# Performance work log

Hardware: AMD Instinct MI355X
Metric: run time of the kernel (lower is better)

The kernel has to match this reference:

```python
import jax, jax.numpy as jnp
import numpy as np

N_NODES = 32
GAT_OUT = 64
LSTM_H = 128
N_CLS = 4
NEG_SLOPE = 0.2


def setup_inputs() -> dict:
    key = jax.random.key(0)
    ks = jax.random.split(key, 12)
    B, T, E = 32, 512, 96
    F, H = GAT_OUT, LSTM_H
    s = 0.05
    return {
        "x_seq": jax.random.normal(ks[0], (B, T, N_NODES), jnp.float32),
        "edge_index": jax.random.randint(ks[1], (2, E), 0, N_NODES, jnp.int32),
        # GATConv params (heads=1): lin weight [in=1, F], attention vectors [F], bias [F]
        "w_gat": jax.random.normal(ks[2], (1, F), jnp.float32) * s,
        "att_src": jax.random.normal(ks[3], (F,), jnp.float32) * s,
        "att_dst": jax.random.normal(ks[4], (F,), jnp.float32) * s,
        "b_gat": jnp.zeros((F,), jnp.float32),
        # LSTM params, torch gate order (i, f, g, o)
        "W_ih": jax.random.normal(ks[5], (N_NODES * F, 4 * H), jnp.float32) * s,
        "W_hh": jax.random.normal(ks[6], (H, 4 * H), jnp.float32) * s,
        "b_ih": jnp.zeros((4 * H,), jnp.float32),
        "b_hh": jnp.zeros((4 * H,), jnp.float32),
        # classifier
        "W_fc": jax.random.normal(ks[7], (H, N_CLS), jnp.float32) * s,
        "b_fc": jnp.zeros((N_CLS,), jnp.float32),
    }


def _forward(x_seq, edge_index, w_gat, att_src, att_dst, b_gat,
             W_ih, W_hh, b_ih, b_hh, W_fc, b_fc):
    B, T, N = x_seq.shape
    F = w_gat.shape[1]
    H = W_hh.shape[0]

    # --- GAT over all (B,T) steps at once (PyG GATConv, heads=1, self-loops) ---
    loops = jnp.arange(N, dtype=edge_index.dtype)
    src = jnp.concatenate([edge_index[0], loops])  # [Et]
    dst = jnp.concatenate([edge_index[1], loops])  # [Et]
    Et = src.shape[0]

    h = x_seq[..., None] * w_gat            # [B,T,N,F] (in_channels=1 linear)
    a_s = h @ att_src                        # [B,T,N]
    a_d = h @ att_dst                        # [B,T,N]
    e = a_s[..., src] + a_d[..., dst]        # [B,T,Et]
    e = jnp.where(e > 0, e, NEG_SLOPE * e)   # LeakyReLU(0.2)

    # segment softmax over destination node, batched over B*T
    e2 = jnp.moveaxis(e, -1, 0).reshape(Et, B * T)
    m = jax.ops.segment_max(e2, dst, num_segments=N)        # [N,B*T]
    ex = jnp.exp(e2 - m[dst])
    z = jax.ops.segment_sum(ex, dst, num_segments=N)        # [N,B*T]
    alpha = ex / z[dst]                                      # [Et,B*T]
    alpha = jnp.moveaxis(alpha.reshape(Et, B, T), 0, -1)     # [B,T,Et]

    msg = alpha[..., None] * h[:, :, src, :]                 # [B,T,Et,F]
    onehot = (dst[:, None] == jnp.arange(N)).astype(h.dtype)  # [Et,N]
    out = jnp.einsum('btef,en->btnf', msg, onehot) + b_gat    # [B,T,N,F]

    seq = out.reshape(B, T, N * F)           # [B,T,2048]

    # --- single-layer LSTM (batch_first), torch gate order i,f,g,o ---
    xw = seq @ W_ih + (b_ih + b_hh)          # [B,T,4H]

    def step(carry, xw_t):
        hs, cs = carry
        g = xw_t + hs @ W_hh                 # [B,4H]
        i, f, gg, o = jnp.split(g, 4, axis=-1)
        cs = jax.nn.sigmoid(f) * cs + jax.nn.sigmoid(i) * jnp.tanh(gg)
        hs = jax.nn.sigmoid(o) * jnp.tanh(cs)
        return (hs, cs), None

    h0 = jnp.zeros((B, H), seq.dtype)
    (h_last, _), _ = jax.lax.scan(step, (h0, h0), jnp.moveaxis(xw, 1, 0))

    return h_last @ W_fc + b_fc              # [B,num_classes]


def reference(x_seq, edge_index, w_gat, att_src, att_dst, b_gat,
              W_ih, W_hh, b_ih, b_hh, W_fc, b_fc):
    return _forward(x_seq, edge_index, w_gat, att_src, att_dst, b_gat,
                    W_ih, W_hh, b_ih, b_hh, W_fc, b_fc)
```

## Files before the change

### kernel.cpp

```cpp
#include <hip/hip_runtime.h>

#define NN 32
#define FF 64
#define HH 128
#define G4 512
#define BB 32
#define TT 512
#define ET 128
#define NPOS (BB*TT)

__device__ __forceinline__ float frcp(float x) { return __builtin_amdgcn_rcpf(x); }

__global__ __launch_bounds__(512) void prep_kernel(const float* __restrict__ w_gat,
                                                   const float* __restrict__ b_gat,
                                                   const float* __restrict__ W_ih,
                                                   const float* __restrict__ W_hh,
                                                   float* __restrict__ W_eff,
                                                   float* __restrict__ biasp,
                                                   float* __restrict__ Wt) {
  int j = threadIdx.x;
  int n = blockIdx.x;
  float accw = 0.f, accb = 0.f;
#pragma unroll 8
  for (int f = 0; f < FF; ++f) {
    float wv = W_ih[(n * FF + f) * G4 + j];
    accw = fmaf(w_gat[f], wv, accw);
    accb = fmaf(b_gat[f], wv, accb);
  }
  W_eff[n * G4 + j] = accw;
  biasp[n * G4 + j] = accb;
  int g0 = (n * G4 + j) * 4;
#pragma unroll
  for (int q = 0; q < 4; ++q) {
    int e = g0 + q;
    int tl = e >> 7, idx = e & 127;
    int r = tl >> 2, kq = tl & 3;
    int g = idx >> 5, kk = idx & 31;
    Wt[e] = W_hh[(kq * 32 + kk) * G4 + g * 128 + r];
  }
}

__global__ __launch_bounds__(256) void gatxw_kernel(const float* __restrict__ x_seq,
                                                    const int* __restrict__ ei,
                                                    const float* __restrict__ w_gat,
                                                    const float* __restrict__ att_src,
                                                    const float* __restrict__ att_dst,
                                                    const float* __restrict__ b_ih,
                                                    const float* __restrict__ b_hh,
                                                    const float* __restrict__ W_eff,
                                                    const float* __restrict__ biasp,
                                                    float* __restrict__ xw) {
  __shared__ int srt[ET];
  __shared__ int offs[NN + 1];
  __shared__ int cnt[NN];
  __shared__ float xs[256];
  __shared__ float sl[256];
  __shared__ float scal_sh[2];
  int tid = threadIdx.x;
  int posbase = blockIdx.x * 8;
  float we0[NN], we1[NN];
#pragma unroll
  for (int nn = 0; nn < NN; ++nn) {
    we0[nn] = W_eff[nn * G4 + tid];
    we1[nn] = W_eff[nn * G4 + 256 + tid];
  }
  float b0 = b_ih[tid] + b_hh[tid];
  float b1 = b_ih[256 + tid] + b_hh[256 + tid];
#pragma unroll 8
  for (int n = 0; n < NN; ++n) {
    b0 += biasp[n * G4 + tid];
    b1 += biasp[n * G4 + 256 + tid];
  }
  if (tid < NN) cnt[tid] = 0;
  __syncthreads();
  int es = 0, ed = 0, tk = 0;
  if (tid < ET) {
    if (tid < 96) { es = ei[tid]; ed = ei[96 + tid]; }
    else { es = tid - 96; ed = tid - 96; }
    tk = atomicAdd(&cnt[ed], 1);
  }
  __syncthreads();
  if (tid == 0) {
    offs[0] = 0;
    for (int n = 0; n < NN; ++n) offs[n + 1] = offs[n] + cnt[n];
  }
  if (tid == 1) {
    float cs = 0.f, cd = 0.f;
    for (int f = 0; f < FF; ++f) {
      cs = fmaf(w_gat[f], att_src[f], cs);
      cd = fmaf(w_gat[f], att_dst[f], cd);
    }
    scal_sh[0] = cs;
    scal_sh[1] = cd;
  }
  __syncthreads();
  if (tid < ET) srt[offs[ed] + tk] = es;
  xs[tid] = x_seq[posbase * NN + tid];
  __syncthreads();
  float cs = scal_sh[0], cd = scal_sh[1];
  int p = tid >> 5, n = tid & 31;
  int base = p * 32;
  int e0 = offs[n], e1 = offs[n + 1];
  float xn = xs[base + n];
  float cdxn = cd * xn;
  float m = -3.0e38f;
  for (int e = e0; e < e1; ++e) {
    float ev = fmaf(cs, xs[base + srt[e]], cdxn);
    ev = ev > 0.f ? ev : 0.2f * ev;
    m = fmaxf(m, ev);
  }
  float z = 0.f, sa = 0.f;
  for (int e = e0; e < e1; ++e) {
    float xsv = xs[base + srt[e]];
    float ev = fmaf(cs, xsv, cdxn);
    ev = ev > 0.f ? ev : 0.2f * ev;
    float ex = __expf(ev - m);
    z += ex;
    sa = fmaf(ex, xsv, sa);
  }
  sl[p * 32 + n] = sa * frcp(z);
  __syncthreads();
  for (int pp = 0; pp < 8; ++pp) {
    const float4* sp = (const float4*)&sl[pp * 32];
    float a0 = b0, a1 = b1;
#pragma unroll
    for (int q = 0; q < 8; ++q) {
      float4 sv = sp[q];
      a0 = fmaf(sv.x, we0[4 * q], a0);
      a0 = fmaf(sv.y, we0[4 * q + 1], a0);
      a0 = fmaf(sv.z, we0[4 * q + 2], a0);
      a0 = fmaf(sv.w, we0[4 * q + 3], a0);
      a1 = fmaf(sv.x, we1[4 * q], a1);
      a1 = fmaf(sv.y, we1[4 * q + 1], a1);
      a1 = fmaf(sv.z, we1[4 * q + 2], a1);
      a1 = fmaf(sv.w, we1[4 * q + 3], a1);
    }
    size_t row = (size_t)(posbase + pp) * G4;
    xw[row + tid] = a0;
    xw[row + 256 + tid] = a1;
  }
}


#define PK16F(HP, W0, W1, W2, W3) \
  "v_pk_fma_f32 v[216:217], v[" HP "], v[" W0 "], 0\n\t" \
  "v_pk_fma_f32 v[218:219], v[" HP "], v[" W1 "], 0\n\t" \
  "v_pk_fma_f32 v[220:221], v[" HP "], v[" W2 "], 0\n\t" \
  "v_pk_fma_f32 v[222:223], v[" HP "], v[" W3 "], 0\n\t"

#define PK16A(HP, W0, W1, W2, W3) \
  "v_pk_fma_f32 v[216:217], v[" HP "], v[" W0 "], v[216:217]\n\t" \
  "v_pk_fma_f32 v[218:219], v[" HP "], v[" W1 "], v[218:219]\n\t" \
  "v_pk_fma_f32 v[220:221], v[" HP "], v[" W2 "], v[220:221]\n\t" \
  "v_pk_fma_f32 v[222:223], v[" HP "], v[" W3 "], v[222:223]\n\t"

#define PHASE(XSLOT, RD, WR) \
  "ds_read_b128 v[32:35], " RD "\n\t" \
  "ds_read_b128 v[36:39], " RD " offset:16\n\t" \
  "ds_read_b128 v[40:43], " RD " offset:32\n\t" \
  "ds_read_b128 v[44:47], " RD " offset:48\n\t" \
  "ds_read_b128 v[48:51], " RD " offset:64\n\t" \
  "ds_read_b128 v[52:55], " RD " offset:80\n\t" \
  "ds_read_b128 v[56:59], " RD " offset:96\n\t" \
  "ds_read_b128 v[60:63], " RD " offset:112\n\t" \
  "s_waitcnt lgkmcnt(7)\n\t" \
  PK16F("32:33", "64:65",  "96:97",   "128:129", "160:161") \
  PK16A("34:35", "66:67",  "98:99",   "130:131", "162:163") \
  "s_waitcnt lgkmcnt(6)\n\t" \
  PK16A("36:37", "68:69",  "100:101", "132:133", "164:165") \
  PK16A("38:39", "70:71",  "102:103", "134:135", "166:167") \
  "s_waitcnt lgkmcnt(5)\n\t" \
  PK16A("40:41", "72:73",  "104:105", "136:137", "168:169") \
  PK16A("42:43", "74:75",  "106:107", "138:139", "170:171") \
  "s_waitcnt lgkmcnt(4)\n\t" \
  PK16A("44:45", "76:77",  "108:109", "140:141", "172:173") \
  PK16A("46:47", "78:79",  "110:111", "142:143", "174:175") \
  "s_waitcnt lgkmcnt(3)\n\t" \
  PK16A("48:49", "80:81",  "112:113", "144:145", "176:177") \
  PK16A("50:51", "82:83",  "114:115", "146:147", "178:179") \
  "s_waitcnt lgkmcnt(2)\n\t" \
  PK16A("52:53", "84:85",  "116:117", "148:149", "180:181") \
  PK16A("54:55", "86:87",  "118:119", "150:151", "182:183") \
  "s_waitcnt lgkmcnt(1)\n\t" \
  PK16A("56:57", "88:89",  "120:121", "152:153", "184:185") \
  PK16A("58:59", "90:91",  "122:123", "154:155", "186:187") \
  "s_waitcnt lgkmcnt(0)\n\t" \
  PK16A("60:61", "92:93",  "124:125", "156:157", "188:189") \
  PK16A("62:63", "94:95",  "126:127", "158:159", "190:191") \
  "s_waitcnt vmcnt(3)\n\t" \
  "v_mov_b32 v215, " XSLOT "\n\t" \
  "global_load_dword " XSLOT ", v194, %[xwb]\n\t" \
  "v_add_u32 v194, 0x800, v194\n\t" \
  "v_add_f32 v204, v216, v217\n\t" \
  "v_add_f32 v205, v218, v219\n\t" \
  "v_add_f32 v206, v220, v221\n\t" \
  "v_add_f32 v207, v222, v223\n\t" \
  "v_add_f32_dpp v204, v204, v204 quad_perm:[1,0,3,2] row_mask:0xf bank_mask:0xf\n\t" \
  "v_add_f32_dpp v205, v205, v205 quad_perm:[1,0,3,2] row_mask:0xf bank_mask:0xf\n\t" \
  "v_add_f32_dpp v206, v206, v206 quad_perm:[1,0,3,2] row_mask:0xf bank_mask:0xf\n\t" \
  "v_add_f32_dpp v207, v207, v207 quad_perm:[1,0,3,2] row_mask:0xf bank_mask:0xf\n\t" \
  "v_add_f32_dpp v204, v204, v204 quad_perm:[2,3,0,1] row_mask:0xf bank_mask:0xf\n\t" \
  "v_add_f32_dpp v205, v205, v205 quad_perm:[2,3,0,1] row_mask:0xf bank_mask:0xf\n\t" \
  "v_add_f32_dpp v206, v206, v206 quad_perm:[2,3,0,1] row_mask:0xf bank_mask:0xf\n\t" \
  "v_add_f32_dpp v207, v207, v207 quad_perm:[2,3,0,1] row_mask:0xf bank_mask:0xf\n\t" \
  "v_cndmask_b32 v208, v204, v205, s[22:23]\n\t" \
  "v_cndmask_b32 v209, v206, v207, s[22:23]\n\t" \
  "v_cndmask_b32 v208, v208, v209, s[24:25]\n\t" \
  "v_add_f32 v208, v208, v215\n\t" \
  "v_mul_f32 v209, v200, v208\n\t" \
  "v_exp_f32 v209, v209\n\t" \
  "s_nop 0\n\t" \
  "v_add_f32 v209, 1.0, v209\n\t" \
  "v_rcp_f32 v209, v209\n\t" \
  "s_nop 0\n\t" \
  "v_fma_f32 v210, v201, v209, v202\n\t" \
  "s_nop 1\n\t" \
  "v_add_f32_dpp v211, v210, v203 quad_perm:[0,0,0,0] row_mask:0xf bank_mask:0xf\n\t" \
  "v_add_f32_dpp v212, v210, v203 quad_perm:[1,1,1,1] row_mask:0xf bank_mask:0xf\n\t" \
  "v_add_f32_dpp v213, v210, v203 quad_perm:[2,2,2,2] row_mask:0xf bank_mask:0xf\n\t" \
  "v_add_f32_dpp v214, v210, v203 quad_perm:[3,3,3,3] row_mask:0xf bank_mask:0xf\n\t" \
  "v_mul_f32 v211, v211, v213\n\t" \
  "v_fma_f32 v199, v212, v199, v211\n\t" \
  "v_mul_f32 v209, 0x4038aa3b, v199\n\t" \
  "v_exp_f32 v209, v209\n\t" \
  "s_nop 0\n\t" \
  "v_add_f32 v209, 1.0, v209\n\t" \
  "v_rcp_f32 v209, v209\n\t" \
  "s_nop 0\n\t" \
  "v_fma_f32 v209, -2.0, v209, 1.0\n\t" \
  "v_mul_f32 v209, v214, v209\n\t" \
  "ds_write_b32 " WR ", v209\n\t" \
  "s_waitcnt lgkmcnt(0)\n\t" \
  "s_barrier\n\t"

__global__ __launch_bounds__(512, 2) void lstm_kernel(const float* __restrict__ xw,
                                                      const float* __restrict__ Wt,
                                                      const float* __restrict__ W_fc,
                                                      const float* __restrict__ b_fc,
                                                      float* __restrict__ out) {
  __shared__ __align__(16) float lds[320];
  int b = blockIdx.x, tid = threadIdx.x;
  int r = tid >> 2, kq = tid & 3;
  if (tid < 320) lds[tid] = 0.f;
  const float* xwb = xw + (size_t)b * TT * G4;
  unsigned xoff0 = (unsigned)((kq * 128 + r) * 4);
  unsigned wtoff = (unsigned)(tid * 512);
  unsigned lbase = (unsigned)(uintptr_t)&lds[0];
  unsigned rda = lbase + kq * 160;
  unsigned rdb = rda + 640;
  unsigned wra = lbase + (((r >> 5) * 40 + (r & 31)) << 2);
  unsigned wrb = wra + 640;
  float kmulf = (kq == 2) ? __uint_as_float(0x4038aa3bu)
                          : __uint_as_float(0xbfb8aa3bu);
  float Af = (kq == 2) ? -2.f : 1.f;
  float Bf = (kq == 2) ? 1.f : 0.f;
  unsigned kqodd = kq & 1, kqhi = kq >> 1;
  __syncthreads();
  asm volatile(
    "v_mov_b32 v194, %[xo]\n\t"
    "v_mov_b32 v195, %[rda]\n\t"
    "v_mov_b32 v196, %[rdb]\n\t"
    "v_mov_b32 v197, %[wra]\n\t"
    "v_mov_b32 v198, %[wrb]\n\t"
    "v_mov_b32 v199, 0\n\t"
    "v_mov_b32 v200, %[km]\n\t"
    "v_mov_b32 v201, %[Aa]\n\t"
    "v_mov_b32 v202, %[Bb]\n\t"
    "v_mov_b32 v203, 0\n\t"
    "v_cmp_eq_u32 s[22:23], 1, %[kodd]\n\t"
    "v_cmp_eq_u32 s[24:25], 1, %[khi]\n\t"
    "global_load_dword v224, v194, %[xwb]\n\t"
    "v_add_u32 v194, 0x800, v194\n\t"
    "global_load_dword v225, v194, %[xwb]\n\t"
    "v_add_u32 v194, 0x800, v194\n\t"
    "global_load_dword v226, v194, %[xwb]\n\t"
    "v_add_u32 v194, 0x800, v194\n\t"
    "global_load_dword v227, v194, %[xwb]\n\t"
    "v_add_u32 v194, 0x800, v194\n\t"
    "global_load_dwordx4 v[64:67], %[wto], %[wtb] offset:0\n\t"
    "global_load_dwordx4 v[68:71], %[wto], %[wtb] offset:16\n\t"
    "global_load_dwordx4 v[72:75], %[wto], %[wtb] offset:32\n\t"
    "global_load_dwordx4 v[76:79], %[wto], %[wtb] offset:48\n\t"
    "global_load_dwordx4 v[80:83], %[wto], %[wtb] offset:64\n\t"
    "global_load_dwordx4 v[84:87], %[wto], %[wtb] offset:80\n\t"
    "global_load_dwordx4 v[88:91], %[wto], %[wtb] offset:96\n\t"
    "global_load_dwordx4 v[92:95], %[wto], %[wtb] offset:112\n\t"
    "global_load_dwordx4 v[96:99], %[wto], %[wtb] offset:128\n\t"
    "global_load_dwordx4 v[100:103], %[wto], %[wtb] offset:144\n\t"
    "global_load_dwordx4 v[104:107], %[wto], %[wtb] offset:160\n\t"
    "global_load_dwordx4 v[108:111], %[wto], %[wtb] offset:176\n\t"
    "global_load_dwordx4 v[112:115], %[wto], %[wtb] offset:192\n\t"
    "global_load_dwordx4 v[116:119], %[wto], %[wtb] offset:208\n\t"
    "global_load_dwordx4 v[120:123], %[wto], %[wtb] offset:224\n\t"
    "global_load_dwordx4 v[124:127], %[wto], %[wtb] offset:240\n\t"
    "global_load_dwordx4 v[128:131], %[wto], %[wtb] offset:256\n\t"
    "global_load_dwordx4 v[132:135], %[wto], %[wtb] offset:272\n\t"
    "global_load_dwordx4 v[136:139], %[wto], %[wtb] offset:288\n\t"
    "global_load_dwordx4 v[140:143], %[wto], %[wtb] offset:304\n\t"
    "global_load_dwordx4 v[144:147], %[wto], %[wtb] offset:320\n\t"
    "global_load_dwordx4 v[148:151], %[wto], %[wtb] offset:336\n\t"
    "global_load_dwordx4 v[152:155], %[wto], %[wtb] offset:352\n\t"
    "global_load_dwordx4 v[156:159], %[wto], %[wtb] offset:368\n\t"
    "global_load_dwordx4 v[160:163], %[wto], %[wtb] offset:384\n\t"
    "global_load_dwordx4 v[164:167], %[wto], %[wtb] offset:400\n\t"
    "global_load_dwordx4 v[168:171], %[wto], %[wtb] offset:416\n\t"
    "global_load_dwordx4 v[172:175], %[wto], %[wtb] offset:432\n\t"
    "global_load_dwordx4 v[176:179], %[wto], %[wtb] offset:448\n\t"
    "global_load_dwordx4 v[180:183], %[wto], %[wtb] offset:464\n\t"
    "global_load_dwordx4 v[184:187], %[wto], %[wtb] offset:480\n\t"
    "global_load_dwordx4 v[188:191], %[wto], %[wtb] offset:496\n\t"
    "s_waitcnt vmcnt(0)\n\t"
    "s_movk_i32 s20, 0x80\n\t"
    "L_lstm_%=:\n\t"
    PHASE("v224", "v195", "v198")
    PHASE("v225", "v196", "v197")
    PHASE("v226", "v195", "v198")
    PHASE("v227", "v196", "v197")
    "s_sub_u32 s20, s20, 1\n\t"
    "s_cmp_lg_u32 s20, 0\n\t"
    "s_cbranch_scc1 L_lstm_%=\n\t"
    "s_waitcnt vmcnt(0) lgkmcnt(0)\n\t"
    :
    : [xwb]"s"(xwb), [wtb]"s"(Wt), [wto]"v"(wtoff), [xo]"v"(xoff0),
      [rda]"v"(rda), [rdb]"v"(rdb), [wra]"v"(wra), [wrb]"v"(wrb),
      [km]"v"(kmulf), [Aa]"v"(Af), [Bb]"v"(Bf),
      [kodd]"v"(kqodd), [khi]"v"(kqhi)
    : "memory", "scc", "s20", "s22", "s23", "s24", "s25",
      "v32","v33","v34","v35","v36","v37","v38","v39",
      "v40","v41","v42","v43","v44","v45","v46","v47",
      "v48","v49","v50","v51","v52","v53","v54","v55",
      "v56","v57","v58","v59","v60","v61","v62","v63",
      "v64","v65","v66","v67","v68","v69","v70","v71",
      "v72","v73","v74","v75","v76","v77","v78","v79",
      "v80","v81","v82","v83","v84","v85","v86","v87",
      "v88","v89","v90","v91","v92","v93","v94","v95",
      "v96","v97","v98","v99","v100","v101","v102","v103",
      "v104","v105","v106","v107","v108","v109","v110","v111",
      "v112","v113","v114","v115","v116","v117","v118","v119",
      "v120","v121","v122","v123","v124","v125","v126","v127",
      "v128","v129","v130","v131","v132","v133","v134","v135",
      "v136","v137","v138","v139","v140","v141","v142","v143",
      "v144","v145","v146","v147","v148","v149","v150","v151",
      "v152","v153","v154","v155","v156","v157","v158","v159",
      "v160","v161","v162","v163","v164","v165","v166","v167",
      "v168","v169","v170","v171","v172","v173","v174","v175",
      "v176","v177","v178","v179","v180","v181","v182","v183",
      "v184","v185","v186","v187","v188","v189","v190","v191",
      "v192","v193","v194","v195","v196","v197","v198","v199",
      "v200","v201","v202","v203","v204","v205","v206","v207",
      "v208","v209","v210","v211","v212","v213","v214","v215",
      "v216","v217","v218","v219","v220","v221","v222","v223",
      "v224","v225","v226","v227");
  __syncthreads();
  if (tid < 4) {
    float acc = b_fc[tid];
#pragma unroll 8
    for (int k = 0; k < HH; ++k)
      acc = fmaf(lds[(k >> 5) * 40 + (k & 31)], W_fc[k * 4 + tid], acc);
    out[b * 4 + tid] = acc;
  }
}

extern "C" void kernel_launch(void* const* d_in, const int* in_sizes, int n_in,
                              void* d_out, int out_size, void* d_ws, size_t ws_size,
                              hipStream_t stream) {
  const float* x_seq   = (const float*)d_in[0];
  const int*   ei      = (const int*)d_in[1];
  const float* w_gat   = (const float*)d_in[2];
  const float* att_src = (const float*)d_in[3];
  const float* att_dst = (const float*)d_in[4];
  const float* b_gat   = (const float*)d_in[5];
  const float* W_ih    = (const float*)d_in[6];
  const float* W_hh    = (const float*)d_in[7];
  const float* b_ih    = (const float*)d_in[8];
  const float* b_hh    = (const float*)d_in[9];
  const float* W_fc    = (const float*)d_in[10];
  const float* b_fc    = (const float*)d_in[11];

  float* ws = (float*)d_ws;
  float* Wt    = ws;
  float* xw    = Wt + 65536;
  float* W_eff = xw + (size_t)(NPOS + 8) * G4;
  float* biasp = W_eff + NN * G4;

  prep_kernel<<<NN, G4, 0, stream>>>(w_gat, b_gat, W_ih, W_hh, W_eff, biasp, Wt);
  gatxw_kernel<<<NPOS / 8, 256, 0, stream>>>(x_seq, ei, w_gat, att_src, att_dst,
                                             b_ih, b_hh, W_eff, biasp, xw);
  lstm_kernel<<<BB, G4, 0, stream>>>(xw, Wt, W_fc, b_fc, (float*)d_out);
}
```

Baseline: 377.2 us.

## Share hidden-state LDS reads across lanes via DPP row rotation in LSTM step

In the LSTM recurrence, each lane now reads only 8 hidden values from LDS per step instead of 32. The other 24 values reach it through three DPP row_ror:4 rotations among neighbouring lanes. The W_hh register layout in prep_kernel is permuted so each rotated slice meets the matching weights, and the LDS hidden-state layout drops its padding. The aim is less LDS read traffic and latency on the serial per-step critical path, at the cost of 24 extra DPP moves per step and a more intricate weight permutation.

```diff
diff --git a/kernel.cpp b/kernel.cpp
--- a/kernel.cpp
+++ b/kernel.cpp
@@ -32,11 +32,17 @@
   int g0 = (n * G4 + j) * 4;
 #pragma unroll
   for (int q = 0; q < 4; ++q) {
-    int e = g0 + q;
-    int tl = e >> 7, idx = e & 127;
-    int r = tl >> 2, kq = tl & 3;
-    int g = idx >> 5, kk = idx & 31;
-    Wt[e] = W_hh[(kq * 32 + kk) * G4 + g * 128 + r];
+    int E = g0 + q;
+    int tl = E >> 7;
+    int idx = E & 127;
+    int s = idx >> 5;
+    int jj = (idx >> 3) & 3;
+    int g = (idx >> 1) & 3;
+    int e = idx & 1;
+    int r = tl >> 2, kq = tl & 3, lr = r & 3;
+    int bb = (lr - s) & 3;
+    int k = kq * 32 + 8 * bb + 2 * jj + e;
+    Wt[E] = W_hh[k * G4 + g * 128 + r];
   }
 }
 
@@ -142,51 +148,52 @@
 }
 
 
-#define PK16F(HP, W0, W1, W2, W3) \
+#define PK4F(HP, W0, W1, W2, W3) \
   "v_pk_fma_f32 v[216:217], v[" HP "], v[" W0 "], 0\n\t" \
   "v_pk_fma_f32 v[218:219], v[" HP "], v[" W1 "], 0\n\t" \
   "v_pk_fma_f32 v[220:221], v[" HP "], v[" W2 "], 0\n\t" \
   "v_pk_fma_f32 v[222:223], v[" HP "], v[" W3 "], 0\n\t"
 
-#define PK16A(HP, W0, W1, W2, W3) \
+#define PK4A(HP, W0, W1, W2, W3) \
   "v_pk_fma_f32 v[216:217], v[" HP "], v[" W0 "], v[216:217]\n\t" \
   "v_pk_fma_f32 v[218:219], v[" HP "], v[" W1 "], v[218:219]\n\t" \
   "v_pk_fma_f32 v[220:221], v[" HP "], v[" W2 "], v[220:221]\n\t" \
   "v_pk_fma_f32 v[222:223], v[" HP "], v[" W3 "], v[222:223]\n\t"
 
+#define ROT8 \
+  "v_mov_b32_dpp v32, v32 row_ror:4 row_mask:0xf bank_mask:0xf\n\t" \
+  "v_mov_b32_dpp v33, v33 row_ror:4 row_mask:0xf bank_mask:0xf\n\t" \
+  "v_mov_b32_dpp v34, v34 row_ror:4 row_mask:0xf bank_mask:0xf\n\t" \
+  "v_mov_b32_dpp v35, v35 row_ror:4 row_mask:0xf bank_mask:0xf\n\t" \
+  "v_mov_b32_dpp v36, v36 row_ror:4 row_mask:0xf bank_mask:0xf\n\t" \
+  "v_mov_b32_dpp v37, v37 row_ror:4 row_mask:0xf bank_mask:0xf\n\t" \
+  "v_mov_b32_dpp v38, v38 row_ror:4 row_mask:0xf bank_mask:0xf\n\t" \
+  "v_mov_b32_dpp v39, v39 row_ror:4 row_mask:0xf bank_mask:0xf\n\t"
+
 #define PHASE(XSLOT, RD, WR) \
   "ds_read_b128 v[32:35], " RD "\n\t" \
   "ds_read_b128 v[36:39], " RD " offset:16\n\t" \
-  "ds_read_b128 v[40:43], " RD " offset:32\n\t" \
-  "ds_read_b128 v[44:47], " RD " offset:48\n\t" \
-  "ds_read_b128 v[48:51], " RD " offset:64\n\t" \
-  "ds_read_b128 v[52:55], " RD " offset:80\n\t" \
-  "ds_read_b128 v[56:59], " RD " offset:96\n\t" \
-  "ds_read_b128 v[60:63], " RD " offset:112\n\t" \
-  "s_waitcnt lgkmcnt(7)\n\t" \
-  PK16F("32:33", "64:65",  "96:97",   "128:129", "160:161") \
-  PK16A("34:35", "66:67",  "98:99",   "130:131", "162:163") \
-  "s_waitcnt lgkmcnt(6)\n\t" \
-  PK16A("36:37", "68:69",  "100:101", "132:133", "164:165") \
-  PK16A("38:39", "70:71",  "102:103", "134:135", "166:167") \
-  "s_waitcnt lgkmcnt(5)\n\t" \
-  PK16A("40:41", "72:73",  "104:105", "136:137", "168:169") \
-  PK16A("42:43", "74:75",  "106:107", "138:139", "170:171") \
-  "s_waitcnt lgkmcnt(4)\n\t" \
-  PK16A("44:45", "76:77",  "108:109", "140:141", "172:173") \
-  PK16A("46:47", "78:79",  "110:111", "142:143", "174:175") \
-  "s_waitcnt lgkmcnt(3)\n\t" \
-  PK16A("48:49", "80:81",  "112:113", "144:145", "176:177") \
-  PK16A("50:51", "82:83",  "114:115", "146:147", "178:179") \
-  "s_waitcnt lgkmcnt(2)\n\t" \
-  PK16A("52:53", "84:85",  "116:117", "148:149", "180:181") \
-  PK16A("54:55", "86:87",  "118:119", "150:151", "182:183") \
   "s_waitcnt lgkmcnt(1)\n\t" \
-  PK16A("56:57", "88:89",  "120:121", "152:153", "184:185") \
-  PK16A("58:59", "90:91",  "122:123", "154:155", "186:187") \
+  PK4F("32:33", "64:65",   "66:67",   "68:69",   "70:71") \
+  PK4A("34:35", "72:73",   "74:75",   "76:77",   "78:79") \
   "s_waitcnt lgkmcnt(0)\n\t" \
-  PK16A("60:61", "92:93",  "124:125", "156:157", "188:189") \
-  PK16A("62:63", "94:95",  "126:127", "158:159", "190:191") \
+  PK4A("36:37", "80:81",   "82:83",   "84:85",   "86:87") \
+  PK4A("38:39", "88:89",   "90:91",   "92:93",   "94:95") \
+  ROT8 \
+  PK4A("32:33", "96:97",   "98:99",   "100:101", "102:103") \
+  PK4A("34:35", "104:105", "106:107", "108:109", "110:111") \
+  PK4A("36:37", "112:113", "114:115", "116:117", "118:119") \
+  PK4A("38:39", "120:121", "122:123", "124:125", "126:127") \
+  ROT8 \
+  PK4A("32:33", "128:129", "130:131", "132:133", "134:135") \
+  PK4A("34:35", "136:137", "138:139", "140:141", "142:143") \
+  PK4A("36:37", "144:145", "146:147", "148:149", "150:151") \
+  PK4A("38:39", "152:153", "154:155", "156:157", "158:159") \
+  ROT8 \
+  PK4A("32:33", "160:161", "162:163", "164:165", "166:167") \
+  PK4A("34:35", "168:169", "170:171", "172:173", "174:175") \
+  PK4A("36:37", "176:177", "178:179", "180:181", "182:183") \
+  PK4A("38:39", "184:185", "186:187", "188:189", "190:191") \
   "s_waitcnt vmcnt(3)\n\t" \
   "v_mov_b32 v215, " XSLOT "\n\t" \
   "global_load_dword " XSLOT ", v194, %[xwb]\n\t" \
@@ -238,18 +245,19 @@
                                                       const float* __restrict__ W_fc,
                                                       const float* __restrict__ b_fc,
                                                       float* __restrict__ out) {
-  __shared__ __align__(16) float lds[320];
+  __shared__ __align__(16) float lds[256];
   int b = blockIdx.x, tid = threadIdx.x;
   int r = tid >> 2, kq = tid & 3;
-  if (tid < 320) lds[tid] = 0.f;
+  int lr = r & 3;
+  if (tid < 256) lds[tid] = 0.f;
   const float* xwb = xw + (size_t)b * TT * G4;
   unsigned xoff0 = (unsigned)((kq * 128 + r) * 4);
   unsigned wtoff = (unsigned)(tid * 512);
   unsigned lbase = (unsigned)(uintptr_t)&lds[0];
-  unsigned rda = lbase + kq * 160;
-  unsigned rdb = rda + 640;
-  unsigned wra = lbase + (((r >> 5) * 40 + (r & 31)) << 2);
-  unsigned wrb = wra + 640;
+  unsigned rda = lbase + (unsigned)(kq * 128 + lr * 32);
+  unsigned rdb = rda + 512;
+  unsigned wra = lbase + (unsigned)(r * 4);
+  unsigned wrb = wra + 512;
   float kmulf = (kq == 2) ? __uint_as_float(0x4038aa3bu)
                           : __uint_as_float(0xbfb8aa3bu);
   float Af = (kq == 2) ? -2.f : 1.f;
@@ -356,7 +364,7 @@
     float acc = b_fc[tid];
 #pragma unroll 8
     for (int k = 0; k < HH; ++k)
-      acc = fmaf(lds[(k >> 5) * 40 + (k & 31)], W_fc[k * 4 + tid], acc);
+      acc = fmaf(lds[k], W_fc[k * 4 + tid], acc);
     out[b * 4 + tid] = acc;
   }
 }
@@ -386,5 +394,5 @@
   prep_kernel<<<NN, G4, 0, stream>>>(w_gat, b_gat, W_ih, W_hh, W_eff, biasp, Wt);
   gatxw_kernel<<<NPOS / 8, 256, 0, stream>>>(x_seq, ei, w_gat, att_src, att_dst,
                                              b_ih, b_hh, W_eff, biasp, xw);
-  lstm_kernel<<<BB, G4, 0, stream>>>(xw, Wt, W_fc, b_fc, (float*)d_out);
+  lstm_kernel<<<BB, 512, 0, stream>>>(xw, Wt, W_fc, b_fc, (float*)d_out);
 }
```

Result: slower. 412.4 us (+9.3%).

## Process two batch sequences per LSTM block, interleaving their recurrences to hide latency

Applied to the files above, without the earlier changes.

Each LSTM workgroup now handles two batch rows and shares the register-resident W_hh slice between them. The gate activation tail of sequence A is interleaved with the packed-FMA matvec of sequence B, so the dependent transcendental and DPP chain of one sequence overlaps the other's arithmetic. The grid is halved to 16 blocks and LDS is doubled to hold both hidden states. This leaves fewer CUs busy and adds more VGPR pressure (up to v252) in exchange for filling the latency bubbles of the serial recurrence.

```diff
diff --git a/kernel.cpp b/kernel.cpp
--- a/kernel.cpp
+++ b/kernel.cpp
@@ -154,7 +154,115 @@
   "v_pk_fma_f32 v[220:221], v[" HP "], v[" W2 "], v[220:221]\n\t" \
   "v_pk_fma_f32 v[222:223], v[" HP "], v[" W3 "], v[222:223]\n\t"
 
-#define PHASE(XSLOT, RD, WR) \
+#define PKB16F(HP, W0, W1, W2, W3) \
+  "v_pk_fma_f32 v[228:229], v[" HP "], v[" W0 "], 0\n\t" \
+  "v_pk_fma_f32 v[230:231], v[" HP "], v[" W1 "], 0\n\t" \
+  "v_pk_fma_f32 v[232:233], v[" HP "], v[" W2 "], 0\n\t" \
+  "v_pk_fma_f32 v[234:235], v[" HP "], v[" W3 "], 0\n\t"
+
+#define PKB16A(HP, W0, W1, W2, W3) \
+  "v_pk_fma_f32 v[228:229], v[" HP "], v[" W0 "], v[228:229]\n\t" \
+  "v_pk_fma_f32 v[230:231], v[" HP "], v[" W1 "], v[230:231]\n\t" \
+  "v_pk_fma_f32 v[232:233], v[" HP "], v[" W2 "], v[232:233]\n\t" \
+  "v_pk_fma_f32 v[234:235], v[" HP "], v[" W3 "], v[234:235]\n\t"
+
+#define ATC1(XSA) \
+  "s_waitcnt vmcnt(7)\n\t" \
+  "v_mov_b32 v215, " XSA "\n\t" \
+  "global_load_dword " XSA ", v194, %[xwa]\n\t" \
+  "v_add_f32 v204, v216, v217\n\t" \
+  "v_add_f32 v205, v218, v219\n\t"
+#define ATC2 \
+  "v_add_f32 v206, v220, v221\n\t" \
+  "v_add_f32 v207, v222, v223\n\t" \
+  "v_add_f32_dpp v204, v204, v204 quad_perm:[1,0,3,2] row_mask:0xf bank_mask:0xf\n\t" \
+  "v_add_f32_dpp v205, v205, v205 quad_perm:[1,0,3,2] row_mask:0xf bank_mask:0xf\n\t" \
+  "v_add_f32_dpp v206, v206, v206 quad_perm:[1,0,3,2] row_mask:0xf bank_mask:0xf\n\t"
+#define ATC3 \
+  "v_add_f32_dpp v207, v207, v207 quad_perm:[1,0,3,2] row_mask:0xf bank_mask:0xf\n\t" \
+  "v_add_f32_dpp v204, v204, v204 quad_perm:[2,3,0,1] row_mask:0xf bank_mask:0xf\n\t" \
+  "v_add_f32_dpp v205, v205, v205 quad_perm:[2,3,0,1] row_mask:0xf bank_mask:0xf\n\t" \
+  "v_add_f32_dpp v206, v206, v206 quad_perm:[2,3,0,1] row_mask:0xf bank_mask:0xf\n\t" \
+  "v_add_f32_dpp v207, v207, v207 quad_perm:[2,3,0,1] row_mask:0xf bank_mask:0xf\n\t"
+#define ATC4 \
+  "v_cndmask_b32 v208, v204, v205, s[22:23]\n\t" \
+  "v_cndmask_b32 v209, v206, v207, s[22:23]\n\t" \
+  "v_cndmask_b32 v208, v208, v209, s[24:25]\n\t" \
+  "v_add_f32 v208, v208, v215\n\t" \
+  "v_mul_f32 v209, v200, v208\n\t"
+#define ATC5 \
+  "v_exp_f32 v209, v209\n\t" \
+  "s_nop 0\n\t" \
+  "v_add_f32 v209, 1.0, v209\n\t" \
+  "v_rcp_f32 v209, v209\n\t" \
+  "s_nop 0\n\t"
+#define ATC6 \
+  "v_fma_f32 v210, v201, v209, v202\n\t" \
+  "s_nop 1\n\t" \
+  "v_add_f32_dpp v211, v210, v203 quad_perm:[0,0,0,0] row_mask:0xf bank_mask:0xf\n\t" \
+  "v_add_f32_dpp v212, v210, v203 quad_perm:[1,1,1,1] row_mask:0xf bank_mask:0xf\n\t" \
+  "v_add_f32_dpp v213, v210, v203 quad_perm:[2,2,2,2] row_mask:0xf bank_mask:0xf\n\t"
+#define ATC7 \
+  "v_add_f32_dpp v214, v210, v203 quad_perm:[3,3,3,3] row_mask:0xf bank_mask:0xf\n\t" \
+  "v_mul_f32 v211, v211, v213\n\t" \
+  "v_fma_f32 v199, v212, v199, v211\n\t" \
+  "v_mul_f32 v209, 0x4038aa3b, v199\n\t"
+#define ATC8(WR) \
+  "v_exp_f32 v209, v209\n\t" \
+  "s_nop 0\n\t" \
+  "v_add_f32 v209, 1.0, v209\n\t" \
+  "v_rcp_f32 v209, v209\n\t" \
+  "s_nop 0\n\t" \
+  "v_fma_f32 v209, -2.0, v209, 1.0\n\t" \
+  "v_mul_f32 v209, v214, v209\n\t" \
+  "ds_write_b32 " WR ", v209\n\t"
+
+#define BTAIL(XSB, WR) \
+  "s_waitcnt vmcnt(7)\n\t" \
+  "v_mov_b32 v241, " XSB "\n\t" \
+  "global_load_dword " XSB ", v194, %[xwb2]\n\t" \
+  "v_add_u32 v194, 0x800, v194\n\t" \
+  "v_add_f32 v242, v228, v229\n\t" \
+  "v_add_f32 v243, v230, v231\n\t" \
+  "v_add_f32 v244, v232, v233\n\t" \
+  "v_add_f32 v245, v234, v235\n\t" \
+  "v_add_f32_dpp v242, v242, v242 quad_perm:[1,0,3,2] row_mask:0xf bank_mask:0xf\n\t" \
+  "v_add_f32_dpp v243, v243, v243 quad_perm:[1,0,3,2] row_mask:0xf bank_mask:0xf\n\t" \
+  "v_add_f32_dpp v244, v244, v244 quad_perm:[1,0,3,2] row_mask:0xf bank_mask:0xf\n\t" \
+  "v_add_f32_dpp v245, v245, v245 quad_perm:[1,0,3,2] row_mask:0xf bank_mask:0xf\n\t" \
+  "v_add_f32_dpp v242, v242, v242 quad_perm:[2,3,0,1] row_mask:0xf bank_mask:0xf\n\t" \
+  "v_add_f32_dpp v243, v243, v243 quad_perm:[2,3,0,1] row_mask:0xf bank_mask:0xf\n\t" \
+  "v_add_f32_dpp v244, v244, v244 quad_perm:[2,3,0,1] row_mask:0xf bank_mask:0xf\n\t" \
+  "v_add_f32_dpp v245, v245, v245 quad_perm:[2,3,0,1] row_mask:0xf bank_mask:0xf\n\t" \
+  "v_cndmask_b32 v246, v242, v243, s[22:23]\n\t" \
+  "v_cndmask_b32 v247, v244, v245, s[22:23]\n\t" \
+  "v_cndmask_b32 v246, v246, v247, s[24:25]\n\t" \
+  "v_add_f32 v246, v246, v241\n\t" \
+  "v_mul_f32 v247, v200, v246\n\t" \
+  "v_exp_f32 v247, v247\n\t" \
+  "s_nop 0\n\t" \
+  "v_add_f32 v247, 1.0, v247\n\t" \
+  "v_rcp_f32 v247, v247\n\t" \
+  "s_nop 0\n\t" \
+  "v_fma_f32 v248, v201, v247, v202\n\t" \
+  "s_nop 1\n\t" \
+  "v_add_f32_dpp v249, v248, v203 quad_perm:[0,0,0,0] row_mask:0xf bank_mask:0xf\n\t" \
+  "v_add_f32_dpp v250, v248, v203 quad_perm:[1,1,1,1] row_mask:0xf bank_mask:0xf\n\t" \
+  "v_add_f32_dpp v251, v248, v203 quad_perm:[2,2,2,2] row_mask:0xf bank_mask:0xf\n\t" \
+  "v_add_f32_dpp v252, v248, v203 quad_perm:[3,3,3,3] row_mask:0xf bank_mask:0xf\n\t" \
+  "v_mul_f32 v249, v249, v251\n\t" \
+  "v_fma_f32 v240, v250, v240, v249\n\t" \
+  "v_mul_f32 v247, 0x4038aa3b, v240\n\t" \
+  "v_exp_f32 v247, v247\n\t" \
+  "s_nop 0\n\t" \
+  "v_add_f32 v247, 1.0, v247\n\t" \
+  "v_rcp_f32 v247, v247\n\t" \
+  "s_nop 0\n\t" \
+  "v_fma_f32 v247, -2.0, v247, 1.0\n\t" \
+  "v_mul_f32 v247, v252, v247\n\t" \
+  "ds_write_b32 " WR ", v247 offset:1280\n\t"
+
+#define PHASE2(XSA, XSB, RD, WR) \
   "ds_read_b128 v[32:35], " RD "\n\t" \
   "ds_read_b128 v[36:39], " RD " offset:16\n\t" \
   "ds_read_b128 v[40:43], " RD " offset:32\n\t" \
@@ -187,49 +295,48 @@
   "s_waitcnt lgkmcnt(0)\n\t" \
   PK16A("60:61", "92:93",  "124:125", "156:157", "188:189") \
   PK16A("62:63", "94:95",  "126:127", "158:159", "190:191") \
-  "s_waitcnt vmcnt(3)\n\t" \
-  "v_mov_b32 v215, " XSLOT "\n\t" \
-  "global_load_dword " XSLOT ", v194, %[xwb]\n\t" \
-  "v_add_u32 v194, 0x800, v194\n\t" \
-  "v_add_f32 v204, v216, v217\n\t" \
-  "v_add_f32 v205, v218, v219\n\t" \
-  "v_add_f32 v206, v220, v221\n\t" \
-  "v_add_f32 v207, v222, v223\n\t" \
-  "v_add_f32_dpp v204, v204, v204 quad_perm:[1,0,3,2] row_mask:0xf bank_mask:0xf\n\t" \
-  "v_add_f32_dpp v205, v205, v205 quad_perm:[1,0,3,2] row_mask:0xf bank_mask:0xf\n\t" \
-  "v_add_f32_dpp v206, v206, v206 quad_perm:[1,0,3,2] row_mask:0xf bank_mask:0xf\n\t" \
-  "v_add_f32_dpp v207, v207, v207 quad_perm:[1,0,3,2] row_mask:0xf bank_mask:0xf\n\t" \
-  "v_add_f32_dpp v204, v204, v204 quad_perm:[2,3,0,1] row_mask:0xf bank_mask:0xf\n\t" \
-  "v_add_f32_dpp v205, v205, v205 quad_perm:[2,3,0,1] row_mask:0xf bank_mask:0xf\n\t" \
-  "v_add_f32_dpp v206, v206, v206 quad_perm:[2,3,0,1] row_mask:0xf bank_mask:0xf\n\t" \
-  "v_add_f32_dpp v207, v207, v207 quad_perm:[2,3,0,1] row_mask:0xf bank_mask:0xf\n\t" \
-  "v_cndmask_b32 v208, v204, v205, s[22:23]\n\t" \
-  "v_cndmask_b32 v209, v206, v207, s[22:23]\n\t" \
-  "v_cndmask_b32 v208, v208, v209, s[24:25]\n\t" \
-  "v_add_f32 v208, v208, v215\n\t" \
-  "v_mul_f32 v209, v200, v208\n\t" \
-  "v_exp_f32 v209, v209\n\t" \
-  "s_nop 0\n\t" \
-  "v_add_f32 v209, 1.0, v209\n\t" \
-  "v_rcp_f32 v209, v209\n\t" \
-  "s_nop 0\n\t" \
-  "v_fma_f32 v210, v201, v209, v202\n\t" \
-  "s_nop 1\n\t" \
-  "v_add_f32_dpp v211, v210, v203 quad_perm:[0,0,0,0] row_mask:0xf bank_mask:0xf\n\t" \
-  "v_add_f32_dpp v212, v210, v203 quad_perm:[1,1,1,1] row_mask:0xf bank_mask:0xf\n\t" \
-  "v_add_f32_dpp v213, v210, v203 quad_perm:[2,2,2,2] row_mask:0xf bank_mask:0xf\n\t" \
-  "v_add_f32_dpp v214, v210, v203 quad_perm:[3,3,3,3] row_mask:0xf bank_mask:0xf\n\t" \
-  "v_mul_f32 v211, v211, v213\n\t" \
-  "v_fma_f32 v199, v212, v199, v211\n\t" \
-  "v_mul_f32 v209, 0x4038aa3b, v199\n\t" \
-  "v_exp_f32 v209, v209\n\t" \
-  "s_nop 0\n\t" \
-  "v_add_f32 v209, 1.0, v209\n\t" \
-  "v_rcp_f32 v209, v209\n\t" \
-  "s_nop 0\n\t" \
-  "v_fma_f32 v209, -2.0, v209, 1.0\n\t" \
-  "v_mul_f32 v209, v214, v209\n\t" \
-  "ds_write_b32 " WR ", v209\n\t" \
+   \
+  "ds_read_b128 v[32:35], " RD " offset:1280\n\t" \
+  "ds_read_b128 v[36:39], " RD " offset:1296\n\t" \
+  "ds_read_b128 v[40:43], " RD " offset:1312\n\t" \
+  "ds_read_b128 v[44:47], " RD " offset:1328\n\t" \
+  "ds_read_b128 v[48:51], " RD " offset:1344\n\t" \
+  "ds_read_b128 v[52:55], " RD " offset:1360\n\t" \
+  "ds_read_b128 v[56:59], " RD " offset:1376\n\t" \
+  "ds_read_b128 v[60:63], " RD " offset:1392\n\t" \
+  ATC1(XSA) \
+  ATC2 \
+  ATC3 \
+  "s_waitcnt lgkmcnt(7)\n\t" \
+  PKB16F("32:33", "64:65",  "96:97",   "128:129", "160:161") \
+  PKB16A("34:35", "66:67",  "98:99",   "130:131", "162:163") \
+  ATC4 \
+  "s_waitcnt lgkmcnt(6)\n\t" \
+  PKB16A("36:37", "68:69",  "100:101", "132:133", "164:165") \
+  PKB16A("38:39", "70:71",  "102:103", "134:135", "166:167") \
+  ATC5 \
+  "s_waitcnt lgkmcnt(5)\n\t" \
+  PKB16A("40:41", "72:73",  "104:105", "136:137", "168:169") \
+  PKB16A("42:43", "74:75",  "106:107", "138:139", "170:171") \
+  ATC6 \
+  "s_waitcnt lgkmcnt(4)\n\t" \
+  PKB16A("44:45", "76:77",  "108:109", "140:141", "172:173") \
+  PKB16A("46:47", "78:79",  "110:111", "142:143", "174:175") \
+  ATC7 \
+  "s_waitcnt lgkmcnt(3)\n\t" \
+  PKB16A("48:49", "80:81",  "112:113", "144:145", "176:177") \
+  PKB16A("50:51", "82:83",  "114:115", "146:147", "178:179") \
+  ATC8(WR) \
+  "s_waitcnt lgkmcnt(2)\n\t" \
+  PKB16A("52:53", "84:85",  "116:117", "148:149", "180:181") \
+  PKB16A("54:55", "86:87",  "118:119", "150:151", "182:183") \
+  "s_waitcnt lgkmcnt(1)\n\t" \
+  PKB16A("56:57", "88:89",  "120:121", "152:153", "184:185") \
+  PKB16A("58:59", "90:91",  "122:123", "154:155", "186:187") \
+  "s_waitcnt lgkmcnt(0)\n\t" \
+  PKB16A("60:61", "92:93",  "124:125", "156:157", "188:189") \
+  PKB16A("62:63", "94:95",  "126:127", "158:159", "190:191") \
+  BTAIL(XSB, WR) \
   "s_waitcnt lgkmcnt(0)\n\t" \
   "s_barrier\n\t"
 
@@ -238,11 +345,12 @@
                                                       const float* __restrict__ W_fc,
                                                       const float* __restrict__ b_fc,
                                                       float* __restrict__ out) {
-  __shared__ __align__(16) float lds[320];
+  __shared__ __align__(16) float lds[640];
   int b = blockIdx.x, tid = threadIdx.x;
   int r = tid >> 2, kq = tid & 3;
-  if (tid < 320) lds[tid] = 0.f;
-  const float* xwb = xw + (size_t)b * TT * G4;
+  for (int i = tid; i < 640; i += 512) lds[i] = 0.f;
+  const float* xwa  = xw + (size_t)(2 * b) * TT * G4;
+  const float* xwb2 = xw + (size_t)(2 * b + 1) * TT * G4;
   unsigned xoff0 = (unsigned)((kq * 128 + r) * 4);
   unsigned wtoff = (unsigned)(tid * 512);
   unsigned lbase = (unsigned)(uintptr_t)&lds[0];
@@ -263,19 +371,24 @@
     "v_mov_b32 v197, %[wra]\n\t"
     "v_mov_b32 v198, %[wrb]\n\t"
     "v_mov_b32 v199, 0\n\t"
+    "v_mov_b32 v240, 0\n\t"
     "v_mov_b32 v200, %[km]\n\t"
     "v_mov_b32 v201, %[Aa]\n\t"
     "v_mov_b32 v202, %[Bb]\n\t"
     "v_mov_b32 v203, 0\n\t"
     "v_cmp_eq_u32 s[22:23], 1, %[kodd]\n\t"
     "v_cmp_eq_u32 s[24:25], 1, %[khi]\n\t"
-    "global_load_dword v224, v194, %[xwb]\n\t"
+    "global_load_dword v224, v194, %[xwa]\n\t"
+    "global_load_dword v236, v194, %[xwb2]\n\t"
     "v_add_u32 v194, 0x800, v194\n\t"
-    "global_load_dword v225, v194, %[xwb]\n\t"
+    "global_load_dword v225, v194, %[xwa]\n\t"
+    "global_load_dword v237, v194, %[xwb2]\n\t"
     "v_add_u32 v194, 0x800, v194\n\t"
-    "global_load_dword v226, v194, %[xwb]\n\t"
+    "global_load_dword v226, v194, %[xwa]\n\t"
+    "global_load_dword v238, v194, %[xwb2]\n\t"
     "v_add_u32 v194, 0x800, v194\n\t"
-    "global_load_dword v227, v194, %[xwb]\n\t"
+    "global_load_dword v227, v194, %[xwa]\n\t"
+    "global_load_dword v239, v194, %[xwb2]\n\t"
     "v_add_u32 v194, 0x800, v194\n\t"
     "global_load_dwordx4 v[64:67], %[wto], %[wtb] offset:0\n\t"
     "global_load_dwordx4 v[68:71], %[wto], %[wtb] offset:16\n\t"
@@ -312,16 +425,16 @@
     "s_waitcnt vmcnt(0)\n\t"
     "s_movk_i32 s20, 0x80\n\t"
     "L_lstm_%=:\n\t"
-    PHASE("v224", "v195", "v198")
-    PHASE("v225", "v196", "v197")
-    PHASE("v226", "v195", "v198")
-    PHASE("v227", "v196", "v197")
+    PHASE2("v224", "v236", "v195", "v198")
+    PHASE2("v225", "v237", "v196", "v197")
+    PHASE2("v226", "v238", "v195", "v198")
+    PHASE2("v227", "v239", "v196", "v197")
     "s_sub_u32 s20, s20, 1\n\t"
     "s_cmp_lg_u32 s20, 0\n\t"
     "s_cbranch_scc1 L_lstm_%=\n\t"
     "s_waitcnt vmcnt(0) lgkmcnt(0)\n\t"
     :
-    : [xwb]"s"(xwb), [wtb]"s"(Wt), [wto]"v"(wtoff), [xo]"v"(xoff0),
+    : [xwa]"s"(xwa), [xwb2]"s"(xwb2), [wtb]"s"(Wt), [wto]"v"(wtoff), [xo]"v"(xoff0),
       [rda]"v"(rda), [rdb]"v"(rdb), [wra]"v"(wra), [wrb]"v"(wrb),
       [km]"v"(kmulf), [Aa]"v"(Af), [Bb]"v"(Bf),
       [kodd]"v"(kqodd), [khi]"v"(kqhi)
@@ -350,14 +463,22 @@
       "v200","v201","v202","v203","v204","v205","v206","v207",
       "v208","v209","v210","v211","v212","v213","v214","v215",
       "v216","v217","v218","v219","v220","v221","v222","v223",
-      "v224","v225","v226","v227");
+      "v224","v225","v226","v227","v228","v229","v230","v231",
+      "v232","v233","v234","v235","v236","v237","v238","v239",
+      "v240","v241","v242","v243","v244","v245","v246","v247",
+      "v248","v249","v250","v251","v252");
   __syncthreads();
   if (tid < 4) {
-    float acc = b_fc[tid];
+    float a0 = b_fc[tid], a1 = b_fc[tid];
 #pragma unroll 8
-    for (int k = 0; k < HH; ++k)
-      acc = fmaf(lds[(k >> 5) * 40 + (k & 31)], W_fc[k * 4 + tid], acc);
-    out[b * 4 + tid] = acc;
+    for (int k = 0; k < HH; ++k) {
+      int li = (k >> 5) * 40 + (k & 31);
+      float wf = W_fc[k * 4 + tid];
+      a0 = fmaf(lds[li], wf, a0);
+      a1 = fmaf(lds[320 + li], wf, a1);
+    }
+    out[(2 * b) * 4 + tid] = a0;
+    out[(2 * b + 1) * 4 + tid] = a1;
   }
 }
 
@@ -386,5 +507,5 @@
   prep_kernel<<<NN, G4, 0, stream>>>(w_gat, b_gat, W_ih, W_hh, W_eff, biasp, Wt);
   gatxw_kernel<<<NPOS / 8, 256, 0, stream>>>(x_seq, ei, w_gat, att_src, att_dst,
                                              b_ih, b_hh, W_eff, biasp, xw);
-  lstm_kernel<<<BB, G4, 0, stream>>>(xw, Wt, W_fc, b_fc, (float*)d_out);
+  lstm_kernel<<<BB / 2, 512, 0, stream>>>(xw, Wt, W_fc, b_fc, (float*)d_out);
 }
```

Result: slower. 594.0 us (+57.5%).
